# Optimization experiments

Hardware: AMD Instinct MI355X
Metric: run time of the kernel (lower is better)

Reference implementation:

```python
import jax, jax.numpy as jnp
import numpy as np

ALPHA, GAMMA = 0.25, 2.0
SPARSITY_PENALTY = 1.0
FOCAL_W, SPARSITY_W, CONC_W = 1.0, 0.8, 1.5
CONC_INNER_W = 1.0  # ConcentrationLoss(concentration_weight=1.0)


def setup_inputs() -> dict:
    key = jax.random.key(0)
    k1, k2 = jax.random.split(key)
    B, C, H, W = 16, 20, 256, 256
    pred = jax.random.normal(k1, (B, C, H, W), dtype=jnp.float32)
    target = (jax.random.uniform(k2, (B, C, H, W)) < 0.05).astype(jnp.float32)
    return {"pred": pred, "target": target}


def reference(pred, target):
    B, C, H, W = pred.shape
    p = jax.nn.sigmoid(pred)

    # ---- Focal loss ----
    is_pos = target == 1.0
    pt = jnp.where(is_pos, p, 1.0 - p)
    alpha_t = jnp.where(is_pos, ALPHA, 1.0 - ALPHA)
    focal = jnp.mean(-alpha_t * (1.0 - pt) ** GAMMA * jnp.log(pt + 1e-8))

    # ---- Sparsity loss ----
    sparsity = jnp.mean((pred - target) ** 2) + SPARSITY_PENALTY * jnp.mean(jnp.abs(pred))

    # ---- Concentration loss (vectorized over (b, c)) ----
    y = jnp.arange(H, dtype=jnp.float32)[:, None]   # [H,1]
    x = jnp.arange(W, dtype=jnp.float32)[None, :]   # [1,W]
    mass = target.sum(axis=(2, 3))                  # [B,C]
    valid = mass > 0
    safe_mass = jnp.where(valid, mass, 1.0)
    cy = jnp.einsum('bchw,hw->bc', target, jnp.broadcast_to(y, (H, W))) / safe_mass
    cx = jnp.einsum('bchw,hw->bc', target, jnp.broadcast_to(x, (H, W))) / safe_mass
    # squared distance to per-(b,c) target centroid: [B,C,H,W]
    dsq = (y[None, None] - cy[:, :, None, None]) ** 2 + (x[None, None] - cx[:, :, None, None]) ** 2
    per_sample = jnp.mean(p * dsq, axis=(2, 3))     # [B,C]
    n_valid = valid.sum()
    conc_sum = jnp.sum(jnp.where(valid, per_sample, 0.0))
    concentration = jnp.where(
        n_valid > 0,
        conc_sum / jnp.maximum(n_valid, 1).astype(jnp.float32),
        0.0,
    ) * CONC_INNER_W

    total = FOCAL_W * focal + SPARSITY_W * sparsity + CONC_W * concentration
    return total, focal, sparsity, concentration
```

## Files before the change

### kernel.cpp

```cpp
#include <hip/hip_runtime.h>
#include <math.h>
#include <stdint.h>

constexpr int Bn = 16, Cn = 20, Hn = 256, Wn = 256;
constexpr int BCn = Bn * Cn;
constexpr int HWn = Hn * Wn;
constexpr int SPLIT = 8;
constexpr int NBLK = BCn * SPLIT;
constexpr int CHUNK = HWn / SPLIT;
constexpr int TPB = 256;
constexpr int ITERS = CHUNK / (TPB * 4);
constexpr int NSLOT = 10;

typedef float f32x4 __attribute__((ext_vector_type(4)));

__device__ inline float wave_reduce(float v) {
    #pragma unroll
    for (int o = 32; o > 0; o >>= 1) v += __shfl_down(v, o, 64);
    return v;
}

__global__ __launch_bounds__(TPB) void partials_kernel(
        const float* __restrict__ pred, const float* __restrict__ target,
        float* __restrict__ ws) {
    const int blk = blockIdx.x;
    const int bc = blk >> 3;
    const int chunk = blk & (SPLIT - 1);
    const long long base = (long long)bc * HWn + (long long)chunk * CHUNK;
    const f32x4* __restrict__ p4 = (const f32x4*)(pred + base);
    const f32x4* __restrict__ t4 = (const f32x4*)(target + base);
    const int tid = threadIdx.x;

    const float x0 = (float)((tid * 4) & 255);
    const float ybase = (float)(chunk * 32 + (tid >> 6));
    constexpr float L2E = 1.44269504088896f;

    float a_mass = 0.f, a_ty = 0.f, a_jt = 0.f, a_p = 0.f, a_py = 0.f,
          a_jp = 0.f, a_pyy = 0.f, a_j2p = 0.f, a_foc = 0.f, a_sq = 0.f,
          a_abs = 0.f;

    #pragma unroll 1
    for (int i = 0; i < ITERS; i++) {
        const int idx = i * TPB + tid;
        const f32x4 pc = __builtin_nontemporal_load(p4 + idx);
        const f32x4 tc = __builtin_nontemporal_load(t4 + idx);
        const float yf = ybase + (float)(i << 2);

        const float pv4[4] = {pc.x, pc.y, pc.z, pc.w};
        const float tv4[4] = {tc.x, tc.y, tc.z, tc.w};
        float st4 = 0.f, sp4 = 0.f;
        #pragma unroll
        for (int j = 0; j < 4; j++) {
            const float v = pv4[j];
            const float t = tv4[j];
            const float u  = v * L2E;
            const float e  = __builtin_amdgcn_exp2f(-u);
            const float p  = __builtin_amdgcn_rcpf(1.0f + e);
            const float l2p = __builtin_amdgcn_logf(p);
            const float l2pt = fmaf(t, u, l2p - u);
            const float om = fmaf(t, fmaf(p, -2.0f, 1.0f), p);
            const float at = fmaf(t, -0.5f, 0.75f);
            a_foc = fmaf(at * l2pt, om * om, a_foc);
            const float d = v - t;
            a_sq = fmaf(d, d, a_sq);
            a_abs += fabsf(v);
            st4 += t;
            sp4 += p;
            if (j == 1)      { a_jt += t;                 a_jp += p;                 a_j2p += p; }
            else if (j == 2) { a_jt = fmaf(t, 2.f, a_jt); a_jp = fmaf(p, 2.f, a_jp); a_j2p = fmaf(p, 4.f, a_j2p); }
            else if (j == 3) { a_jt = fmaf(t, 3.f, a_jt); a_jp = fmaf(p, 3.f, a_jp); a_j2p = fmaf(p, 9.f, a_j2p); }
        }
        a_mass += st4;
        a_ty  = fmaf(st4, yf, a_ty);
        a_p   += sp4;
        a_py  = fmaf(sp4, yf, a_py);
        a_pyy = fmaf(sp4, yf * yf, a_pyy);
    }

    float slot[NSLOT];
    slot[0] = a_mass;
    slot[1] = a_ty;
    slot[2] = fmaf(x0, a_mass, a_jt);
    slot[3] = a_p;
    slot[4] = a_py;
    slot[5] = fmaf(x0, a_p, a_jp);
    slot[6] = a_pyy + x0 * x0 * a_p + 2.f * x0 * a_jp + a_j2p;
    slot[7] = a_foc;
    slot[8] = a_sq;
    slot[9] = a_abs;

    __shared__ float red[TPB / 64][NSLOT];
    const int lane = tid & 63, wave = tid >> 6;
    #pragma unroll
    for (int k = 0; k < NSLOT; k++) {
        const float r = wave_reduce(slot[k]);
        if (lane == 0) red[wave][k] = r;
    }
    __syncthreads();
    if (tid < NSLOT) {
        float s = 0.f;
        #pragma unroll
        for (int w = 0; w < TPB / 64; w++) s += red[w][tid];
        ws[tid * NBLK + blk] = s;
    }
}

__global__ __launch_bounds__(320) void finalize_kernel(
        const float* __restrict__ ws, float* __restrict__ out) {
    const int tid = threadIdx.x;
    const float4* __restrict__ w4 = (const float4*)ws;

    float s[NSLOT];
    #pragma unroll
    for (int k = 0; k < NSLOT; k++) {
        float a = 0.f;
        #pragma unroll
        for (int q = 0; q < SPLIT / 4; q++) {
            const float4 v = w4[k * (NBLK / 4) + tid * (SPLIT / 4) + q];
            a += v.x + v.y + v.z + v.w;
        }
        s[k] = a;
    }

    const float mass = s[0];
    const bool valid = mass > 0.f;
    const float sm = valid ? mass : 1.0f;
    const float cy = s[1] / sm, cx = s[2] / sm;
    const float pdsq = s[6] - 2.f * cy * s[4] - 2.f * cx * s[5]
                     + (cy * cy + cx * cx) * s[3];
    float vals[5];
    vals[0] = valid ? (pdsq / (float)HWn) : 0.f;
    vals[1] = valid ? 1.f : 0.f;
    vals[2] = s[7];
    vals[3] = s[8];
    vals[4] = s[9];

    __shared__ float lds[5][5];
    const int lane = tid & 63, wave = tid >> 6;
    #pragma unroll
    for (int k = 0; k < 5; k++) {
        const float r = wave_reduce(vals[k]);
        if (lane == 0) lds[wave][k] = r;
    }
    __syncthreads();

    if (tid == 0) {
        float tot[5];
        #pragma unroll
        for (int k = 0; k < 5; k++) {
            float a = 0.f;
            #pragma unroll
            for (int w = 0; w < 5; w++) a += lds[w][k];
            tot[k] = a;
        }
        const float NTOT = (float)Bn * Cn * Hn * Wn;
        constexpr float LN2 = 0.69314718055994531f;
        const float focal = -LN2 * tot[2] / NTOT;
        const float sparsity = tot[3] / NTOT + tot[4] / NTOT;
        const float concentration =
            (tot[1] > 0.f) ? (tot[0] / fmaxf(tot[1], 1.f)) : 0.f;
        const float total = 1.0f * focal + 0.8f * sparsity + 1.5f * concentration;
        out[0] = total;
        out[1] = focal;
        out[2] = sparsity;
        out[3] = concentration;
    }
}

extern "C" void kernel_launch(void* const* d_in, const int* in_sizes, int n_in,
                              void* d_out, int out_size, void* d_ws, size_t ws_size,
                              hipStream_t stream) {
    const float* pred   = (const float*)d_in[0];
    const float* target = (const float*)d_in[1];
    float* out = (float*)d_out;
    float* ws  = (float*)d_ws;

    partials_kernel<<<NBLK, TPB, 0, stream>>>(pred, target, ws);
    finalize_kernel<<<1, 320, 0, stream>>>(ws, out);
}
```

Baseline: 172.4 us.

## Halve block split and software-pipeline loads with a four-deep register prefetch

Cuts the number of blocks per (b,c) plane from 8 to 4, so each block handles 64 rows, and updates the finalize kernel to read one float4 per plane. The main loop now keeps four pairs of pred/target vector loads in flight in registers, processing one pair while issuing the next load. The goal is more memory-level parallelism per wave to hide HBM latency in this bandwidth-bound reduction. The cost is higher register pressure and fewer blocks (1280), which could reduce occupancy or leave the GPU less evenly loaded.

```diff
diff --git a/kernel.cpp b/kernel.cpp
--- a/kernel.cpp
+++ b/kernel.cpp
@@ -5,7 +5,7 @@
 constexpr int Bn = 16, Cn = 20, Hn = 256, Wn = 256;
 constexpr int BCn = Bn * Cn;
 constexpr int HWn = Hn * Wn;
-constexpr int SPLIT = 8;
+constexpr int SPLIT = 4;
 constexpr int NBLK = BCn * SPLIT;
 constexpr int CHUNK = HWn / SPLIT;
 constexpr int TPB = 256;
@@ -24,7 +24,7 @@
         const float* __restrict__ pred, const float* __restrict__ target,
         float* __restrict__ ws) {
     const int blk = blockIdx.x;
-    const int bc = blk >> 3;
+    const int bc = blk >> 2;
     const int chunk = blk & (SPLIT - 1);
     const long long base = (long long)bc * HWn + (long long)chunk * CHUNK;
     const f32x4* __restrict__ p4 = (const f32x4*)(pred + base);
@@ -32,20 +32,14 @@
     const int tid = threadIdx.x;
 
     const float x0 = (float)((tid * 4) & 255);
-    const float ybase = (float)(chunk * 32 + (tid >> 6));
+    float yf = (float)(chunk * 64 + (tid >> 6));
     constexpr float L2E = 1.44269504088896f;
 
     float a_mass = 0.f, a_ty = 0.f, a_jt = 0.f, a_p = 0.f, a_py = 0.f,
           a_jp = 0.f, a_pyy = 0.f, a_j2p = 0.f, a_foc = 0.f, a_sq = 0.f,
           a_abs = 0.f;
 
-    #pragma unroll 1
-    for (int i = 0; i < ITERS; i++) {
-        const int idx = i * TPB + tid;
-        const f32x4 pc = __builtin_nontemporal_load(p4 + idx);
-        const f32x4 tc = __builtin_nontemporal_load(t4 + idx);
-        const float yf = ybase + (float)(i << 2);
-
+    auto PROC = [&](const f32x4& pc, const f32x4& tc) {
         const float pv4[4] = {pc.x, pc.y, pc.z, pc.w};
         const float tv4[4] = {tc.x, tc.y, tc.z, tc.w};
         float st4 = 0.f, sp4 = 0.f;
@@ -75,7 +69,35 @@
         a_p   += sp4;
         a_py  = fmaf(sp4, yf, a_py);
         a_pyy = fmaf(sp4, yf * yf, a_pyy);
+        yf += 4.0f;
+    };
+
+    f32x4 P0 = __builtin_nontemporal_load(p4 + 0 * TPB + tid);
+    f32x4 T0 = __builtin_nontemporal_load(t4 + 0 * TPB + tid);
+    f32x4 P1 = __builtin_nontemporal_load(p4 + 1 * TPB + tid);
+    f32x4 T1 = __builtin_nontemporal_load(t4 + 1 * TPB + tid);
+    f32x4 P2 = __builtin_nontemporal_load(p4 + 2 * TPB + tid);
+    f32x4 T2 = __builtin_nontemporal_load(t4 + 2 * TPB + tid);
+    f32x4 P3 = __builtin_nontemporal_load(p4 + 3 * TPB + tid);
+    f32x4 T3 = __builtin_nontemporal_load(t4 + 3 * TPB + tid);
+
+    int i = 0;
+    #pragma unroll 1
+    for (; i + 4 < ITERS; i += 4) {
+        PROC(P0, T0);
+        P0 = __builtin_nontemporal_load(p4 + (i + 4) * TPB + tid);
+        T0 = __builtin_nontemporal_load(t4 + (i + 4) * TPB + tid);
+        PROC(P1, T1);
+        P1 = __builtin_nontemporal_load(p4 + (i + 5) * TPB + tid);
+        T1 = __builtin_nontemporal_load(t4 + (i + 5) * TPB + tid);
+        PROC(P2, T2);
+        P2 = __builtin_nontemporal_load(p4 + (i + 6) * TPB + tid);
+        T2 = __builtin_nontemporal_load(t4 + (i + 6) * TPB + tid);
+        PROC(P3, T3);
+        P3 = __builtin_nontemporal_load(p4 + (i + 7) * TPB + tid);
+        T3 = __builtin_nontemporal_load(t4 + (i + 7) * TPB + tid);
     }
+    PROC(P0, T0); PROC(P1, T1); PROC(P2, T2); PROC(P3, T3);
 
     float slot[NSLOT];
     slot[0] = a_mass;
@@ -113,13 +135,8 @@
     float s[NSLOT];
     #pragma unroll
     for (int k = 0; k < NSLOT; k++) {
-        float a = 0.f;
-        #pragma unroll
-        for (int q = 0; q < SPLIT / 4; q++) {
-            const float4 v = w4[k * (NBLK / 4) + tid * (SPLIT / 4) + q];
-            a += v.x + v.y + v.z + v.w;
-        }
-        s[k] = a;
+        const float4 v = w4[k * (NBLK / 4) + tid];
+        s[k] = v.x + v.y + v.z + v.w;
     }
 
     const float mass = s[0];
```

New measurement: 169.8 us (median of 2 runs). No clear change (-1.5%).
